# Kernel optimization log

Measured on AMD Instinct MI355X. Metric: run time of the kernel, lower is better.

Reference implementation:

```python
import jax, jax.numpy as jnp
import numpy as np

HIDDEN = 1024
FFN = 4096
N_EXPERTS = 8
TOP_K = 2


def setup_inputs() -> dict:
    key = jax.random.key(0)
    ks = jax.random.split(key, 6)
    x = jax.random.normal(ks[0], (2, 2048, HIDDEN), dtype=jnp.float32)
    Wr = jax.random.normal(ks[1], (N_EXPERTS, HIDDEN), dtype=jnp.float32) * 0.02
    W1 = jax.random.normal(ks[2], (N_EXPERTS, FFN, HIDDEN), dtype=jnp.float32) * 0.02
    b1 = jnp.zeros((N_EXPERTS, FFN), dtype=jnp.float32)
    W2 = jax.random.normal(ks[3], (N_EXPERTS, HIDDEN, FFN), dtype=jnp.float32) * 0.02
    b2 = jnp.zeros((N_EXPERTS, HIDDEN), dtype=jnp.float32)
    return {"x": x, "Wr": Wr, "W1": W1, "b1": b1, "W2": W2, "b2": b2}


def reference(x, Wr, W1, b1, W2, b2):
    # x: [B, S, D]; Wr: [E, D]; W1: [E, F, D]; W2: [E, D, F]
    B, S, D = x.shape
    E = Wr.shape[0]
    xf = x.reshape(-1, D)                              # [T, D]
    T = xf.shape[0]
    logits = xf @ Wr.T                                 # [T, E]
    probs = jax.nn.softmax(logits, axis=-1)
    top_v, top_i = jax.lax.top_k(probs, TOP_K)         # [T, K]
    top_v = top_v / jnp.sum(top_v, axis=-1, keepdims=True)
    # combine weights: zero except the top-k experts per token
    comb = jnp.zeros((T, E), dtype=xf.dtype).at[jnp.arange(T)[:, None], top_i].add(top_v)
    # run every expert densely (same math as gather/FFN/weighted-scatter)
    h = jax.nn.gelu(jnp.einsum('td,efd->etf', xf, W1) + b1[:, None, :], approximate=False)  # [E, T, F]
    y = jnp.einsum('etf,edf->etd', h, W2) + b2[:, None, :]                                   # [E, T, D]
    out = jnp.einsum('etd,te->td', y, comb)            # weighted combine
    return out.reshape(B, S, D)
```

## Files before the change

### kernel.cpp

```cpp
#include <hip/hip_runtime.h>

#define HIDDEN 1024
#define FFN    4096
#define NEXP   8
#define TOKENS 4096
#define ASSIGN 8192
#define NENT   72

typedef __attribute__((ext_vector_type(8))) short s8v;
typedef __attribute__((ext_vector_type(4))) float f4v;

__device__ __forceinline__ float bf2f(ushort u) {
    return __uint_as_float(((unsigned int)u) << 16);
}
__device__ __forceinline__ ushort f2bf(float f) {
    unsigned int x = __float_as_uint(f);
    return (ushort)((x + 0x7fffu + ((x >> 16) & 1u)) >> 16);
}

__device__ __forceinline__ float gelu_f(float v) {
    const float u = v * 0.70710678118654752f;
    const float a = fabsf(u);
    const float t = 1.0f / fmaf(0.3275911f, a, 1.0f);
    const float p = t * (0.254829592f + t * (-0.284496736f + t * (1.421413741f +
                     t * (-1.453152027f + t * 1.061405429f))));
    const float ex = __expf(-u * u);
    float er = 1.0f - p * ex;
    er = (u < 0.f) ? -er : er;
    return 0.5f * v * (1.0f + er);
}

#define GLDS16(g, l) __builtin_amdgcn_global_load_lds( \
    (const __attribute__((address_space(1))) unsigned int*)(g), \
    (__attribute__((address_space(3))) unsigned int*)(l), 16, 0, 0)

__device__ __forceinline__ int swz_scol(int t) {
    const int srow = t >> 2, c = t & 3;
    return ((c ^ ((srow >> 1) & 3)) << 3);
}
__device__ __forceinline__ int lds_off(int row, int lq) {
    return row * 32 + ((lq ^ ((row >> 1) & 3)) << 3);
}

#define KBODY(it, bA, bB, sA, sB)                                               \
  {                                                                             \
    if ((it) == NT - 1)      { asm volatile("s_waitcnt vmcnt(0)" ::: "memory");}\
    else if ((it) == NT - 2) { asm volatile("s_waitcnt vmcnt(4)" ::: "memory");}\
    else                     { asm volatile("s_waitcnt vmcnt(8)" ::: "memory");}\
    __builtin_amdgcn_s_barrier();                                               \
    __builtin_amdgcn_sched_barrier(0);                                          \
    if ((it) + 3 < NT) {                                                        \
      const int kn_ = ((it) + 3) * 32;                                          \
      GLDS16(gA0 + kn_, (sA) + wv * 512);                                       \
      GLDS16(gA1 + kn_, (sA) + 2048 + wv * 512);                                \
      GLDS16(gB0 + kn_, (sB) + wv * 512);                                       \
      GLDS16(gB1 + kn_, (sB) + 2048 + wv * 512);                                \
    }                                                                           \
    s8v a_[4], b_[4];                                                           \
    _Pragma("unroll")                                                           \
    for (int i_ = 0; i_ < 4; ++i_)                                              \
      a_[i_] = *(const s8v*)((bA) + lds_off(row_off + i_ * 16 + l15, lq));      \
    _Pragma("unroll")                                                           \
    for (int j_ = 0; j_ < 4; ++j_)                                              \
      b_[j_] = *(const s8v*)((bB) + lds_off(col_off + j_ * 16 + l15, lq));      \
    __builtin_amdgcn_s_setprio(1);                                              \
    _Pragma("unroll")                                                           \
    for (int i_ = 0; i_ < 4; ++i_)                                              \
      _Pragma("unroll")                                                         \
      for (int j_ = 0; j_ < 4; ++j_)                                            \
        acc[i_][j_] = __builtin_amdgcn_mfma_f32_16x16x32_bf16(a_[i_], b_[j_],   \
                                                              acc[i_][j_], 0, 0, 0); \
    __builtin_amdgcn_s_setprio(0);                                              \
  }

__global__ void conv_kernel(const float4* __restrict__ src, ushort4* __restrict__ dst) {
    const int i = blockIdx.x * blockDim.x + threadIdx.x;
    const float4 v = src[i];
    ushort4 o;
    o.x = f2bf(v.x); o.y = f2bf(v.y); o.z = f2bf(v.z); o.w = f2bf(v.w);
    dst[i] = o;
}

__global__ void router_kernel(const float* __restrict__ x, const float* __restrict__ Wr,
                              int* __restrict__ counts, int* __restrict__ topk_idx,
                              float* __restrict__ topk_w) {
    const int tok  = blockIdx.x;
    const int lane = threadIdx.x;
    float acc[NEXP];
#pragma unroll
    for (int e = 0; e < NEXP; ++e) acc[e] = 0.f;
#pragma unroll
    for (int i = 0; i < HIDDEN / 64; ++i) {
        const int idx = i * 64 + lane;
        const float xv = x[(size_t)tok * HIDDEN + idx];
#pragma unroll
        for (int e = 0; e < NEXP; ++e) acc[e] += xv * Wr[e * HIDDEN + idx];
    }
#pragma unroll
    for (int e = 0; e < NEXP; ++e) {
#pragma unroll
        for (int off = 32; off > 0; off >>= 1) acc[e] += __shfl_xor(acc[e], off);
    }
    if (lane == 0) {
        int i0 = 0;
        for (int e = 1; e < NEXP; ++e) if (acc[e] > acc[i0]) i0 = e;
        int i1 = (i0 == 0) ? 1 : 0;
        for (int e = 0; e < NEXP; ++e) if (e != i0 && acc[e] > acc[i1]) i1 = e;
        const float e1 = expf(acc[i1] - acc[i0]);
        const float s  = 1.f + e1;
        topk_idx[tok * 2 + 0] = i0;
        topk_idx[tok * 2 + 1] = i1;
        topk_w[tok * 2 + 0]   = 1.f / s;
        topk_w[tok * 2 + 1]   = e1 / s;
        atomicAdd(&counts[i0], 1);
        atomicAdd(&counts[i1], 1);
    }
}

__global__ void prefix_kernel(const int* __restrict__ counts, int* __restrict__ offsets,
                              int* __restrict__ cursors, int* __restrict__ tiles) {
    if (threadIdx.x == 0) {
        int s = 0, nt = 0;
        for (int e = 0; e < NEXP; ++e) {
            offsets[e] = s; cursors[e] = s;
            const int ne = counts[e];
            for (int tm = 0; tm * 128 < ne; ++tm) tiles[nt++] = e | (tm << 8);
            s += ne;
        }
        offsets[NEXP] = s;
        for (; nt < NENT; ++nt) tiles[nt] = -1;
    }
}

__global__ void scatter_kernel(const int* __restrict__ topk_idx, const float* __restrict__ topk_w,
                               int* __restrict__ cursors, int* __restrict__ token_list,
                               float* __restrict__ weight_list) {
    const int a = blockIdx.x * blockDim.x + threadIdx.x;
    if (a >= ASSIGN) return;
    const int e   = topk_idx[a];
    const int pos = atomicAdd(&cursors[e], 1);
    token_list[pos]  = a >> 1;
    weight_list[pos] = topk_w[a];
}

__global__ __launch_bounds__(256)
void gemm1_kernel(const ushort* __restrict__ x, const ushort* __restrict__ W1,
                  const float* __restrict__ b1, const int* __restrict__ token_list,
                  const int* __restrict__ counts, const int* __restrict__ offsets,
                  const int* __restrict__ tiles, ushort* __restrict__ h) {
    const int info = tiles[blockIdx.x];
    if (info < 0) return;
    const int e      = info & 255;
    const int tile_m = info >> 8;
    const int tile_n = blockIdx.y;
    const int n_e    = counts[e];
    const int base   = offsets[e];

    __shared__ __align__(16) ushort As[4 * 128 * 32];
    __shared__ __align__(16) ushort Bs[4 * 128 * 32];

    const int t    = threadIdx.x;
    const int lane = t & 63;
    const int wv   = t >> 6;
    const int srow = t >> 2;
    const int scol = swz_scol(t);

    const int r0 = tile_m * 128 + srow;
    const int r1 = r0 + 64;
    const int tokA0 = token_list[base + (r0 < n_e ? r0 : n_e - 1)];
    const int tokA1 = token_list[base + (r1 < n_e ? r1 : n_e - 1)];
    const ushort* gA0 = x + (size_t)tokA0 * HIDDEN + scol;
    const ushort* gA1 = x + (size_t)tokA1 * HIDDEN + scol;
    const ushort* gB0 = W1 + ((size_t)e * FFN + tile_n * 128 + srow) * HIDDEN + scol;
    const ushort* gB1 = W1 + ((size_t)e * FFN + tile_n * 128 + 64 + srow) * HIDDEN + scol;

    f4v acc[4][4];
#pragma unroll
    for (int i = 0; i < 4; ++i)
#pragma unroll
        for (int j = 0; j < 4; ++j) { f4v z = {0.f, 0.f, 0.f, 0.f}; acc[i][j] = z; }

    const int row_off = (wv & 1) * 64;
    const int col_off = (wv >> 1) * 64;
    const int l15 = lane & 15;
    const int lq  = lane >> 4;

    const int NT = HIDDEN / 32;

#pragma unroll
    for (int p = 0; p < 3; ++p) {
        GLDS16(gA0 + p * 32, As + p * 4096 + wv * 512);
        GLDS16(gA1 + p * 32, As + p * 4096 + 2048 + wv * 512);
        GLDS16(gB0 + p * 32, Bs + p * 4096 + wv * 512);
        GLDS16(gB1 + p * 32, Bs + p * 4096 + 2048 + wv * 512);
    }

    for (int it0 = 0; it0 < NT; it0 += 4) {
        KBODY(it0 + 0, As + 0 * 4096, Bs + 0 * 4096, As + 3 * 4096, Bs + 3 * 4096);
        KBODY(it0 + 1, As + 1 * 4096, Bs + 1 * 4096, As + 0 * 4096, Bs + 0 * 4096);
        KBODY(it0 + 2, As + 2 * 4096, Bs + 2 * 4096, As + 1 * 4096, Bs + 1 * 4096);
        KBODY(it0 + 3, As + 3 * 4096, Bs + 3 * 4096, As + 2 * 4096, Bs + 2 * 4096);
    }

    const int mrem = n_e - tile_m * 128;
#pragma unroll
    for (int i = 0; i < 4; ++i) {
#pragma unroll
        for (int rr = 0; rr < 4; ++rr) {
            const int m_loc = row_off + i * 16 + lq * 4 + rr;
            if (m_loc < mrem) {
                const size_t hrow = (size_t)(base + tile_m * 128 + m_loc) * FFN;
#pragma unroll
                for (int j = 0; j < 4; ++j) {
                    const int colF = tile_n * 128 + col_off + j * 16 + l15;
                    const float v = gelu_f(acc[i][j][rr] + b1[e * FFN + colF]);
                    h[hrow + colF] = f2bf(v);
                }
            }
        }
    }
}

__global__ __launch_bounds__(256)
void gemm2_kernel(const ushort* __restrict__ h, const ushort* __restrict__ W2,
                  const float* __restrict__ b2, const float* __restrict__ weight_list,
                  const int* __restrict__ token_list, const int* __restrict__ counts,
                  const int* __restrict__ offsets, const int* __restrict__ tiles,
                  float* __restrict__ out) {
    const int info = tiles[blockIdx.x];
    if (info < 0) return;
    const int e      = info & 255;
    const int tile_m = info >> 8;
    const int tile_n = blockIdx.y;
    const int n_e    = counts[e];
    const int base   = offsets[e];

    __shared__ __align__(16) ushort As[4 * 128 * 32];
    __shared__ __align__(16) ushort Bs[4 * 128 * 32];

    const int t    = threadIdx.x;
    const int lane = t & 63;
    const int wv   = t >> 6;
    const int srow = t >> 2;
    const int scol = swz_scol(t);

    const int r0 = tile_m * 128 + srow;
    const int r1 = r0 + 64;
    const int slot0 = base + (r0 < n_e ? r0 : n_e - 1);
    const int slot1 = base + (r1 < n_e ? r1 : n_e - 1);
    const ushort* gA0 = h + (size_t)slot0 * FFN + scol;
    const ushort* gA1 = h + (size_t)slot1 * FFN + scol;
    const ushort* gB0 = W2 + ((size_t)e * HIDDEN + tile_n * 128 + srow) * FFN + scol;
    const ushort* gB1 = W2 + ((size_t)e * HIDDEN + tile_n * 128 + 64 + srow) * FFN + scol;

    f4v acc[4][4];
#pragma unroll
    for (int i = 0; i < 4; ++i)
#pragma unroll
        for (int j = 0; j < 4; ++j) { f4v z = {0.f, 0.f, 0.f, 0.f}; acc[i][j] = z; }

    const int row_off = (wv & 1) * 64;
    const int col_off = (wv >> 1) * 64;
    const int l15 = lane & 15;
    const int lq  = lane >> 4;

    const int NT = FFN / 32;

#pragma unroll
    for (int p = 0; p < 3; ++p) {
        GLDS16(gA0 + p * 32, As + p * 4096 + wv * 512);
        GLDS16(gA1 + p * 32, As + p * 4096 + 2048 + wv * 512);
        GLDS16(gB0 + p * 32, Bs + p * 4096 + wv * 512);
        GLDS16(gB1 + p * 32, Bs + p * 4096 + 2048 + wv * 512);
    }

    for (int it0 = 0; it0 < NT; it0 += 4) {
        KBODY(it0 + 0, As + 0 * 4096, Bs + 0 * 4096, As + 3 * 4096, Bs + 3 * 4096);
        KBODY(it0 + 1, As + 1 * 4096, Bs + 1 * 4096, As + 0 * 4096, Bs + 0 * 4096);
        KBODY(it0 + 2, As + 2 * 4096, Bs + 2 * 4096, As + 1 * 4096, Bs + 1 * 4096);
        KBODY(it0 + 3, As + 3 * 4096, Bs + 3 * 4096, As + 2 * 4096, Bs + 2 * 4096);
    }

    const int mrem = n_e - tile_m * 128;
#pragma unroll
    for (int i = 0; i < 4; ++i) {
#pragma unroll
        for (int rr = 0; rr < 4; ++rr) {
            const int m_loc = row_off + i * 16 + lq * 4 + rr;
            if (m_loc < mrem) {
                const int slot  = base + tile_m * 128 + m_loc;
                const float wgt = weight_list[slot];
                const int   tok = token_list[slot];
#pragma unroll
                for (int j = 0; j < 4; ++j) {
                    const int colD = tile_n * 128 + col_off + j * 16 + l15;
                    const float v = acc[i][j][rr] + b2[e * HIDDEN + colD];
                    atomicAdd(&out[(size_t)tok * HIDDEN + colD], v * wgt);
                }
            }
        }
    }
}

extern "C" void kernel_launch(void* const* d_in, const int* in_sizes, int n_in,
                              void* d_out, int out_size, void* d_ws, size_t ws_size,
                              hipStream_t stream) {
    const float* x  = (const float*)d_in[0];
    const float* Wr = (const float*)d_in[1];
    const float* W1 = (const float*)d_in[2];
    const float* b1 = (const float*)d_in[3];
    const float* W2 = (const float*)d_in[4];
    const float* b2 = (const float*)d_in[5];
    float* out = (float*)d_out;

    char* ws = (char*)d_ws;
    int*    counts      = (int*)(ws + 0);
    int*    offsets     = (int*)(ws + 256);
    int*    cursors     = (int*)(ws + 512);
    int*    tiles       = (int*)(ws + 768);
    int*    topk_idx    = (int*)(ws + 2048);
    float*  topk_w      = (float*)(ws + 2048 + 32768);
    int*    token_list  = (int*)(ws + 2048 + 65536);
    float*  weight_list = (float*)(ws + 2048 + 98304);
    ushort* x_bf        = (ushort*)(ws + (1 << 20));
    ushort* wbuf        = (ushort*)(ws + (1 << 20) + 8388608);
    ushort* h           = (ushort*)(ws + (1 << 20) + 8388608 + 67108864);

    const int NW = NEXP * FFN * HIDDEN;

    hipMemsetAsync(counts, 0, 64, stream);
    hipMemsetAsync(out, 0, (size_t)TOKENS * HIDDEN * 4, stream);
    conv_kernel<<<(TOKENS * HIDDEN / 4) / 256, 256, 0, stream>>>((const float4*)x, (ushort4*)x_bf);
    conv_kernel<<<(NW / 4) / 256, 256, 0, stream>>>((const float4*)W1, (ushort4*)wbuf);

    router_kernel<<<TOKENS, 64, 0, stream>>>(x, Wr, counts, topk_idx, topk_w);
    prefix_kernel<<<1, 64, 0, stream>>>(counts, offsets, cursors, tiles);
    scatter_kernel<<<ASSIGN / 256, 256, 0, stream>>>(topk_idx, topk_w, cursors,
                                                     token_list, weight_list);

    gemm1_kernel<<<dim3(NENT, FFN / 128), 256, 0, stream>>>(
        x_bf, wbuf, b1, token_list, counts, offsets, tiles, h);

    conv_kernel<<<(NW / 4) / 256, 256, 0, stream>>>((const float4*)W2, (ushort4*)wbuf);

    gemm2_kernel<<<dim3(NENT, HIDDEN / 128), 256, 0, stream>>>(
        h, wbuf, b2, weight_list, token_list, counts, offsets, tiles, out);
}
```

Baseline: 811.6 us.

## Enlarge GEMM tiles to 256 rows, replace atomic combine with bf16 staging

```diff
diff --git a/kernel.cpp b/kernel.cpp
--- a/kernel.cpp
+++ b/kernel.cpp
@@ -5,7 +5,7 @@
 #define NEXP   8
 #define TOKENS 4096
 #define ASSIGN 8192
-#define NENT   72
+#define NENT   40
 
 typedef __attribute__((ext_vector_type(8))) short s8v;
 typedef __attribute__((ext_vector_type(4))) float f4v;
@@ -35,43 +35,11 @@
     (__attribute__((address_space(3))) unsigned int*)(l), 16, 0, 0)
 
 __device__ __forceinline__ int swz_scol(int t) {
-    const int srow = t >> 2, c = t & 3;
-    return ((c ^ ((srow >> 1) & 3)) << 3);
+    return (((t & 3) ^ ((t >> 3) & 3)) << 3);
 }
 __device__ __forceinline__ int lds_off(int row, int lq) {
     return row * 32 + ((lq ^ ((row >> 1) & 3)) << 3);
 }
-
-#define KBODY(it, bA, bB, sA, sB)                                               \
-  {                                                                             \
-    if ((it) == NT - 1)      { asm volatile("s_waitcnt vmcnt(0)" ::: "memory");}\
-    else if ((it) == NT - 2) { asm volatile("s_waitcnt vmcnt(4)" ::: "memory");}\
-    else                     { asm volatile("s_waitcnt vmcnt(8)" ::: "memory");}\
-    __builtin_amdgcn_s_barrier();                                               \
-    __builtin_amdgcn_sched_barrier(0);                                          \
-    if ((it) + 3 < NT) {                                                        \
-      const int kn_ = ((it) + 3) * 32;                                          \
-      GLDS16(gA0 + kn_, (sA) + wv * 512);                                       \
-      GLDS16(gA1 + kn_, (sA) + 2048 + wv * 512);                                \
-      GLDS16(gB0 + kn_, (sB) + wv * 512);                                       \
-      GLDS16(gB1 + kn_, (sB) + 2048 + wv * 512);                                \
-    }                                                                           \
-    s8v a_[4], b_[4];                                                           \
-    _Pragma("unroll")                                                           \
-    for (int i_ = 0; i_ < 4; ++i_)                                              \
-      a_[i_] = *(const s8v*)((bA) + lds_off(row_off + i_ * 16 + l15, lq));      \
-    _Pragma("unroll")                                                           \
-    for (int j_ = 0; j_ < 4; ++j_)                                              \
-      b_[j_] = *(const s8v*)((bB) + lds_off(col_off + j_ * 16 + l15, lq));      \
-    __builtin_amdgcn_s_setprio(1);                                              \
-    _Pragma("unroll")                                                           \
-    for (int i_ = 0; i_ < 4; ++i_)                                              \
-      _Pragma("unroll")                                                         \
-      for (int j_ = 0; j_ < 4; ++j_)                                            \
-        acc[i_][j_] = __builtin_amdgcn_mfma_f32_16x16x32_bf16(a_[i_], b_[j_],   \
-                                                              acc[i_][j_], 0, 0, 0); \
-    __builtin_amdgcn_s_setprio(0);                                              \
-  }
 
 __global__ void conv_kernel(const float4* __restrict__ src, ushort4* __restrict__ dst) {
     const int i = blockIdx.x * blockDim.x + threadIdx.x;
@@ -83,7 +51,7 @@
 
 __global__ void router_kernel(const float* __restrict__ x, const float* __restrict__ Wr,
                               int* __restrict__ counts, int* __restrict__ topk_idx,
-                              float* __restrict__ topk_w) {
+                              float* __restrict__ topk_w, ushort* __restrict__ x_bf) {
     const int tok  = blockIdx.x;
     const int lane = threadIdx.x;
     float acc[NEXP];
@@ -93,6 +61,7 @@
     for (int i = 0; i < HIDDEN / 64; ++i) {
         const int idx = i * 64 + lane;
         const float xv = x[(size_t)tok * HIDDEN + idx];
+        x_bf[(size_t)tok * HIDDEN + idx] = f2bf(xv);
 #pragma unroll
         for (int e = 0; e < NEXP; ++e) acc[e] += xv * Wr[e * HIDDEN + idx];
     }
@@ -124,7 +93,7 @@
         for (int e = 0; e < NEXP; ++e) {
             offsets[e] = s; cursors[e] = s;
             const int ne = counts[e];
-            for (int tm = 0; tm * 128 < ne; ++tm) tiles[nt++] = e | (tm << 8);
+            for (int tm = 0; tm * 256 < ne; ++tm) tiles[nt++] = e | (tm << 8);
             s += ne;
         }
         offsets[NEXP] = s;
@@ -134,85 +103,127 @@
 
 __global__ void scatter_kernel(const int* __restrict__ topk_idx, const float* __restrict__ topk_w,
                                int* __restrict__ cursors, int* __restrict__ token_list,
-                               float* __restrict__ weight_list) {
+                               float* __restrict__ weight_list, int* __restrict__ slot_of) {
     const int a = blockIdx.x * blockDim.x + threadIdx.x;
     if (a >= ASSIGN) return;
     const int e   = topk_idx[a];
     const int pos = atomicAdd(&cursors[e], 1);
     token_list[pos]  = a >> 1;
     weight_list[pos] = topk_w[a];
-}
-
-__global__ __launch_bounds__(256)
+    slot_of[a]       = pos;
+}
+
+#define G1_TILE(T, CA, CB, SA, SB)                                              \
+  if ((T) < NT) {                                                               \
+    if ((T) + 2 < NT) {                                                         \
+      const int kn_ = ((T) + 2) * 32;                                           \
+      GLDS16(gA0 + kn_, (SA) + wv * 512);                                       \
+      GLDS16(gA1 + kn_, (SA) + 4096 + wv * 512);                                \
+      GLDS16(gB0 + kn_, (SB) + wv * 512);                                       \
+      GLDS16(gB1 + kn_, (SB) + 4096 + wv * 512);                                \
+    }                                                                           \
+    s8v a_[4], b_[4], c_[4];                                                    \
+    _Pragma("unroll")                                                           \
+    for (int i_ = 0; i_ < 4; ++i_)                                              \
+      a_[i_] = *(const s8v*)((CA) + lds_off(wm * 128 + i_ * 16 + l15, lq));     \
+    _Pragma("unroll")                                                           \
+    for (int j_ = 0; j_ < 4; ++j_)                                              \
+      b_[j_] = *(const s8v*)((CB) + lds_off(wn * 64 + j_ * 16 + l15, lq));      \
+    _Pragma("unroll")                                                           \
+    for (int i_ = 0; i_ < 4; ++i_)                                              \
+      c_[i_] = *(const s8v*)((CA) + lds_off(wm * 128 + 64 + i_ * 16 + l15, lq));\
+    __builtin_amdgcn_s_setprio(1);                                              \
+    _Pragma("unroll")                                                           \
+    for (int i_ = 0; i_ < 4; ++i_)                                              \
+      _Pragma("unroll")                                                         \
+      for (int j_ = 0; j_ < 4; ++j_)                                            \
+        acc[i_][j_] = __builtin_amdgcn_mfma_f32_16x16x32_bf16(a_[i_], b_[j_],   \
+                                                              acc[i_][j_], 0, 0, 0); \
+    _Pragma("unroll")                                                           \
+    for (int i_ = 0; i_ < 4; ++i_)                                              \
+      _Pragma("unroll")                                                         \
+      for (int j_ = 0; j_ < 4; ++j_)                                            \
+        acc[4 + i_][j_] = __builtin_amdgcn_mfma_f32_16x16x32_bf16(c_[i_], b_[j_], \
+                                                              acc[4 + i_][j_], 0, 0, 0); \
+    __builtin_amdgcn_s_setprio(0);                                              \
+    if ((T) >= NT - 2) { asm volatile("s_waitcnt vmcnt(0)" ::: "memory"); }     \
+    else               { asm volatile("s_waitcnt vmcnt(4)" ::: "memory"); }     \
+    __builtin_amdgcn_s_barrier();                                               \
+    __builtin_amdgcn_sched_barrier(0);                                          \
+  }
+
+__global__ __launch_bounds__(512, 2)
 void gemm1_kernel(const ushort* __restrict__ x, const ushort* __restrict__ W1,
                   const float* __restrict__ b1, const int* __restrict__ token_list,
                   const int* __restrict__ counts, const int* __restrict__ offsets,
                   const int* __restrict__ tiles, ushort* __restrict__ h) {
-    const int info = tiles[blockIdx.x];
+    const int info = tiles[blockIdx.y];
     if (info < 0) return;
     const int e      = info & 255;
     const int tile_m = info >> 8;
-    const int tile_n = blockIdx.y;
+    const int tile_n = blockIdx.x;
     const int n_e    = counts[e];
     const int base   = offsets[e];
 
-    __shared__ __align__(16) ushort As[4 * 128 * 32];
-    __shared__ __align__(16) ushort Bs[4 * 128 * 32];
+    __shared__ __align__(16) ushort As[3 * 256 * 32];
+    __shared__ __align__(16) ushort Bs[3 * 256 * 32];
 
     const int t    = threadIdx.x;
+    const int wv   = t >> 6;
     const int lane = t & 63;
-    const int wv   = t >> 6;
     const int srow = t >> 2;
     const int scol = swz_scol(t);
 
-    const int r0 = tile_m * 128 + srow;
-    const int r1 = r0 + 64;
+    const int r0 = tile_m * 256 + srow;
+    const int r1 = r0 + 128;
     const int tokA0 = token_list[base + (r0 < n_e ? r0 : n_e - 1)];
     const int tokA1 = token_list[base + (r1 < n_e ? r1 : n_e - 1)];
     const ushort* gA0 = x + (size_t)tokA0 * HIDDEN + scol;
     const ushort* gA1 = x + (size_t)tokA1 * HIDDEN + scol;
-    const ushort* gB0 = W1 + ((size_t)e * FFN + tile_n * 128 + srow) * HIDDEN + scol;
-    const ushort* gB1 = W1 + ((size_t)e * FFN + tile_n * 128 + 64 + srow) * HIDDEN + scol;
-
-    f4v acc[4][4];
-#pragma unroll
-    for (int i = 0; i < 4; ++i)
+    const ushort* gB0 = W1 + ((size_t)e * FFN + tile_n * 256 + srow) * HIDDEN + scol;
+    const ushort* gB1 = W1 + ((size_t)e * FFN + tile_n * 256 + 128 + srow) * HIDDEN + scol;
+
+    f4v acc[8][4];
+#pragma unroll
+    for (int i = 0; i < 8; ++i)
 #pragma unroll
         for (int j = 0; j < 4; ++j) { f4v z = {0.f, 0.f, 0.f, 0.f}; acc[i][j] = z; }
 
-    const int row_off = (wv & 1) * 64;
-    const int col_off = (wv >> 1) * 64;
+    const int wm  = wv >> 2;
+    const int wn  = wv & 3;
     const int l15 = lane & 15;
     const int lq  = lane >> 4;
 
     const int NT = HIDDEN / 32;
 
 #pragma unroll
-    for (int p = 0; p < 3; ++p) {
-        GLDS16(gA0 + p * 32, As + p * 4096 + wv * 512);
-        GLDS16(gA1 + p * 32, As + p * 4096 + 2048 + wv * 512);
-        GLDS16(gB0 + p * 32, Bs + p * 4096 + wv * 512);
-        GLDS16(gB1 + p * 32, Bs + p * 4096 + 2048 + wv * 512);
-    }
-
-    for (int it0 = 0; it0 < NT; it0 += 4) {
-        KBODY(it0 + 0, As + 0 * 4096, Bs + 0 * 4096, As + 3 * 4096, Bs + 3 * 4096);
-        KBODY(it0 + 1, As + 1 * 4096, Bs + 1 * 4096, As + 0 * 4096, Bs + 0 * 4096);
-        KBODY(it0 + 2, As + 2 * 4096, Bs + 2 * 4096, As + 1 * 4096, Bs + 1 * 4096);
-        KBODY(it0 + 3, As + 3 * 4096, Bs + 3 * 4096, As + 2 * 4096, Bs + 2 * 4096);
-    }
-
-    const int mrem = n_e - tile_m * 128;
-#pragma unroll
-    for (int i = 0; i < 4; ++i) {
+    for (int p = 0; p < 2; ++p) {
+        GLDS16(gA0 + p * 32, As + p * 8192 + wv * 512);
+        GLDS16(gA1 + p * 32, As + p * 8192 + 4096 + wv * 512);
+        GLDS16(gB0 + p * 32, Bs + p * 8192 + wv * 512);
+        GLDS16(gB1 + p * 32, Bs + p * 8192 + 4096 + wv * 512);
+    }
+    asm volatile("s_waitcnt vmcnt(4)" ::: "memory");
+    __builtin_amdgcn_s_barrier();
+    __builtin_amdgcn_sched_barrier(0);
+
+    for (int t0 = 0; t0 < NT; t0 += 3) {
+        G1_TILE(t0 + 0, As + 0 * 8192, Bs + 0 * 8192, As + 2 * 8192, Bs + 2 * 8192);
+        G1_TILE(t0 + 1, As + 1 * 8192, Bs + 1 * 8192, As + 0 * 8192, Bs + 0 * 8192);
+        G1_TILE(t0 + 2, As + 2 * 8192, Bs + 2 * 8192, As + 1 * 8192, Bs + 1 * 8192);
+    }
+
+    const int mrem = n_e - tile_m * 256;
+#pragma unroll
+    for (int i = 0; i < 8; ++i) {
 #pragma unroll
         for (int rr = 0; rr < 4; ++rr) {
-            const int m_loc = row_off + i * 16 + lq * 4 + rr;
+            const int m_loc = wm * 128 + i * 16 + lq * 4 + rr;
             if (m_loc < mrem) {
-                const size_t hrow = (size_t)(base + tile_m * 128 + m_loc) * FFN;
+                const size_t hrow = (size_t)(base + tile_m * 256 + m_loc) * FFN;
 #pragma unroll
                 for (int j = 0; j < 4; ++j) {
-                    const int colF = tile_n * 128 + col_off + j * 16 + l15;
+                    const int colF = tile_n * 256 + wn * 64 + j * 16 + l15;
                     const float v = gelu_f(acc[i][j][rr] + b1[e * FFN + colF]);
                     h[hrow + colF] = f2bf(v);
                 }
@@ -221,85 +232,138 @@
     }
 }
 
-__global__ __launch_bounds__(256)
+#define G2_TILE(T, CA, CB, SA, SB)                                              \
+  if ((T) < NT) {                                                               \
+    if ((T) + 2 < NT) {                                                         \
+      const int kn_ = ((T) + 2) * 32;                                           \
+      GLDS16(gA0 + kn_, (SA) + wv * 512);                                       \
+      GLDS16(gA1 + kn_, (SA) + 4096 + wv * 512);                                \
+      GLDS16(gB0 + kn_, (SB) + wv * 512);                                       \
+    }                                                                           \
+    s8v a_[4], b_[2], c_[4];                                                    \
+    _Pragma("unroll")                                                           \
+    for (int i_ = 0; i_ < 4; ++i_)                                              \
+      a_[i_] = *(const s8v*)((CA) + lds_off(wm * 128 + i_ * 16 + l15, lq));     \
+    _Pragma("unroll")                                                           \
+    for (int j_ = 0; j_ < 2; ++j_)                                              \
+      b_[j_] = *(const s8v*)((CB) + lds_off(wn * 32 + j_ * 16 + l15, lq));      \
+    _Pragma("unroll")                                                           \
+    for (int i_ = 0; i_ < 4; ++i_)                                              \
+      c_[i_] = *(const s8v*)((CA) + lds_off(wm * 128 + 64 + i_ * 16 + l15, lq));\
+    __builtin_amdgcn_s_setprio(1);                                              \
+    _Pragma("unroll")                                                           \
+    for (int i_ = 0; i_ < 4; ++i_)                                              \
+      _Pragma("unroll")                                                         \
+      for (int j_ = 0; j_ < 2; ++j_)                                            \
+        acc[i_][j_] = __builtin_amdgcn_mfma_f32_16x16x32_bf16(a_[i_], b_[j_],   \
+                                                              acc[i_][j_], 0, 0, 0); \
+    _Pragma("unroll")                                                           \
+    for (int i_ = 0; i_ < 4; ++i_)                                              \
+      _Pragma("unroll")                                                         \
+      for (int j_ = 0; j_ < 2; ++j_)                                            \
+        acc[4 + i_][j_] = __builtin_amdgcn_mfma_f32_16x16x32_bf16(c_[i_], b_[j_], \
+                                                              acc[4 + i_][j_], 0, 0, 0); \
+    __builtin_amdgcn_s_setprio(0);                                              \
+    if ((T) >= NT - 2) { asm volatile("s_waitcnt vmcnt(0)" ::: "memory"); }     \
+    else               { asm volatile("s_waitcnt vmcnt(3)" ::: "memory"); }     \
+    __builtin_amdgcn_s_barrier();                                               \
+    __builtin_amdgcn_sched_barrier(0);                                          \
+  }
+
+__global__ __launch_bounds__(512, 2)
 void gemm2_kernel(const ushort* __restrict__ h, const ushort* __restrict__ W2,
                   const float* __restrict__ b2, const float* __restrict__ weight_list,
-                  const int* __restrict__ token_list, const int* __restrict__ counts,
-                  const int* __restrict__ offsets, const int* __restrict__ tiles,
-                  float* __restrict__ out) {
-    const int info = tiles[blockIdx.x];
+                  const int* __restrict__ counts, const int* __restrict__ offsets,
+                  const int* __restrict__ tiles, ushort* __restrict__ y) {
+    const int info = tiles[blockIdx.y];
     if (info < 0) return;
     const int e      = info & 255;
     const int tile_m = info >> 8;
-    const int tile_n = blockIdx.y;
+    const int tile_n = blockIdx.x;
     const int n_e    = counts[e];
     const int base   = offsets[e];
 
-    __shared__ __align__(16) ushort As[4 * 128 * 32];
-    __shared__ __align__(16) ushort Bs[4 * 128 * 32];
+    __shared__ __align__(16) ushort As[3 * 256 * 32];
+    __shared__ __align__(16) ushort Bs[3 * 128 * 32];
 
     const int t    = threadIdx.x;
+    const int wv   = t >> 6;
     const int lane = t & 63;
-    const int wv   = t >> 6;
     const int srow = t >> 2;
     const int scol = swz_scol(t);
 
-    const int r0 = tile_m * 128 + srow;
-    const int r1 = r0 + 64;
+    const int r0 = tile_m * 256 + srow;
+    const int r1 = r0 + 128;
     const int slot0 = base + (r0 < n_e ? r0 : n_e - 1);
     const int slot1 = base + (r1 < n_e ? r1 : n_e - 1);
     const ushort* gA0 = h + (size_t)slot0 * FFN + scol;
     const ushort* gA1 = h + (size_t)slot1 * FFN + scol;
     const ushort* gB0 = W2 + ((size_t)e * HIDDEN + tile_n * 128 + srow) * FFN + scol;
-    const ushort* gB1 = W2 + ((size_t)e * HIDDEN + tile_n * 128 + 64 + srow) * FFN + scol;
-
-    f4v acc[4][4];
-#pragma unroll
-    for (int i = 0; i < 4; ++i)
-#pragma unroll
-        for (int j = 0; j < 4; ++j) { f4v z = {0.f, 0.f, 0.f, 0.f}; acc[i][j] = z; }
-
-    const int row_off = (wv & 1) * 64;
-    const int col_off = (wv >> 1) * 64;
+
+    f4v acc[8][2];
+#pragma unroll
+    for (int i = 0; i < 8; ++i)
+#pragma unroll
+        for (int j = 0; j < 2; ++j) { f4v z = {0.f, 0.f, 0.f, 0.f}; acc[i][j] = z; }
+
+    const int wm  = wv >> 2;
+    const int wn  = wv & 3;
     const int l15 = lane & 15;
     const int lq  = lane >> 4;
 
     const int NT = FFN / 32;
 
 #pragma unroll
-    for (int p = 0; p < 3; ++p) {
-        GLDS16(gA0 + p * 32, As + p * 4096 + wv * 512);
-        GLDS16(gA1 + p * 32, As + p * 4096 + 2048 + wv * 512);
+    for (int p = 0; p < 2; ++p) {
+        GLDS16(gA0 + p * 32, As + p * 8192 + wv * 512);
+        GLDS16(gA1 + p * 32, As + p * 8192 + 4096 + wv * 512);
         GLDS16(gB0 + p * 32, Bs + p * 4096 + wv * 512);
-        GLDS16(gB1 + p * 32, Bs + p * 4096 + 2048 + wv * 512);
-    }
-
-    for (int it0 = 0; it0 < NT; it0 += 4) {
-        KBODY(it0 + 0, As + 0 * 4096, Bs + 0 * 4096, As + 3 * 4096, Bs + 3 * 4096);
-        KBODY(it0 + 1, As + 1 * 4096, Bs + 1 * 4096, As + 0 * 4096, Bs + 0 * 4096);
-        KBODY(it0 + 2, As + 2 * 4096, Bs + 2 * 4096, As + 1 * 4096, Bs + 1 * 4096);
-        KBODY(it0 + 3, As + 3 * 4096, Bs + 3 * 4096, As + 2 * 4096, Bs + 2 * 4096);
-    }
-
-    const int mrem = n_e - tile_m * 128;
-#pragma unroll
-    for (int i = 0; i < 4; ++i) {
+    }
+    asm volatile("s_waitcnt vmcnt(3)" ::: "memory");
+    __builtin_amdgcn_s_barrier();
+    __builtin_amdgcn_sched_barrier(0);
+
+    for (int t0 = 0; t0 < NT; t0 += 3) {
+        G2_TILE(t0 + 0, As + 0 * 8192, Bs + 0 * 4096, As + 2 * 8192, Bs + 2 * 4096);
+        G2_TILE(t0 + 1, As + 1 * 8192, Bs + 1 * 4096, As + 0 * 8192, Bs + 0 * 4096);
+        G2_TILE(t0 + 2, As + 2 * 8192, Bs + 2 * 4096, As + 1 * 8192, Bs + 1 * 4096);
+    }
+
+    const int mrem = n_e - tile_m * 256;
+#pragma unroll
+    for (int i = 0; i < 8; ++i) {
 #pragma unroll
         for (int rr = 0; rr < 4; ++rr) {
-            const int m_loc = row_off + i * 16 + lq * 4 + rr;
+            const int m_loc = wm * 128 + i * 16 + lq * 4 + rr;
             if (m_loc < mrem) {
-                const int slot  = base + tile_m * 128 + m_loc;
+                const int slot  = base + tile_m * 256 + m_loc;
                 const float wgt = weight_list[slot];
-                const int   tok = token_list[slot];
-#pragma unroll
-                for (int j = 0; j < 4; ++j) {
-                    const int colD = tile_n * 128 + col_off + j * 16 + l15;
+#pragma unroll
+                for (int j = 0; j < 2; ++j) {
+                    const int colD = tile_n * 128 + wn * 32 + j * 16 + l15;
                     const float v = acc[i][j][rr] + b2[e * HIDDEN + colD];
-                    atomicAdd(&out[(size_t)tok * HIDDEN + colD], v * wgt);
+                    y[(size_t)slot * HIDDEN + colD] = f2bf(v * wgt);
                 }
             }
         }
     }
+}
+
+__global__ void combine_kernel(const int* __restrict__ slot_of, const ushort* __restrict__ y,
+                               float* __restrict__ out) {
+    const int idx = blockIdx.x * blockDim.x + threadIdx.x;
+    const int t = idx >> 8;
+    const int d = (idx & 255) * 4;
+    const int s0 = slot_of[t * 2 + 0];
+    const int s1 = slot_of[t * 2 + 1];
+    const ushort4 a = *(const ushort4*)(y + (size_t)s0 * HIDDEN + d);
+    const ushort4 b = *(const ushort4*)(y + (size_t)s1 * HIDDEN + d);
+    float4 o;
+    o.x = bf2f(a.x) + bf2f(b.x);
+    o.y = bf2f(a.y) + bf2f(b.y);
+    o.z = bf2f(a.z) + bf2f(b.z);
+    o.w = bf2f(a.w) + bf2f(b.w);
+    *(float4*)(out + (size_t)t * HIDDEN + d) = o;
 }
 
 extern "C" void kernel_launch(void* const* d_in, const int* in_sizes, int n_in,
@@ -320,29 +384,31 @@
     int*    tiles       = (int*)(ws + 768);
     int*    topk_idx    = (int*)(ws + 2048);
     float*  topk_w      = (float*)(ws + 2048 + 32768);
-    int*    token_list  = (int*)(ws + 2048 + 65536);
-    float*  weight_list = (float*)(ws + 2048 + 98304);
+    int*    slot_of     = (int*)(ws + 2048 + 65536);
+    int*    token_list  = (int*)(ws + 2048 + 98304);
+    float*  weight_list = (float*)(ws + 2048 + 131072);
     ushort* x_bf        = (ushort*)(ws + (1 << 20));
     ushort* wbuf        = (ushort*)(ws + (1 << 20) + 8388608);
     ushort* h           = (ushort*)(ws + (1 << 20) + 8388608 + 67108864);
+    ushort* y           = (ushort*)(ws + (1 << 20) + 8388608 + 2 * 67108864ull);
 
     const int NW = NEXP * FFN * HIDDEN;
 
     hipMemsetAsync(counts, 0, 64, stream);
-    hipMemsetAsync(out, 0, (size_t)TOKENS * HIDDEN * 4, stream);
-    conv_kernel<<<(TOKENS * HIDDEN / 4) / 256, 256, 0, stream>>>((const float4*)x, (ushort4*)x_bf);
+    router_kernel<<<TOKENS, 64, 0, stream>>>(x, Wr, counts, topk_idx, topk_w, x_bf);
     conv_kernel<<<(NW / 4) / 256, 256, 0, stream>>>((const float4*)W1, (ushort4*)wbuf);
 
-    router_kernel<<<TOKENS, 64, 0, stream>>>(x, Wr, counts, topk_idx, topk_w);
     prefix_kernel<<<1, 64, 0, stream>>>(counts, offsets, cursors, tiles);
     scatter_kernel<<<ASSIGN / 256, 256, 0, stream>>>(topk_idx, topk_w, cursors,
-                                                     token_list, weight_list);
-
-    gemm1_kernel<<<dim3(NENT, FFN / 128), 256, 0, stream>>>(
+                                                     token_list, weight_list, slot_of);
+
+    gemm1_kernel<<<dim3(FFN / 256, NENT), 512, 0, stream>>>(
         x_bf, wbuf, b1, token_list, counts, offsets, tiles, h);
 
     conv_kernel<<<(NW / 4) / 256, 256, 0, stream>>>((const float4*)W2, (ushort4*)wbuf);
 
-    gemm2_kernel<<<dim3(NENT, HIDDEN / 128), 256, 0, stream>>>(
-        h, wbuf, b2, weight_list, token_list, counts, offsets, tiles, out);
-}
+    gemm2_kernel<<<dim3(HIDDEN / 128, NENT), 512, 0, stream>>>(
+        h, wbuf, b2, weight_list, counts, offsets, tiles, y);
+
+    combine_kernel<<<(TOKENS * HIDDEN / 4) / 256, 256, 0, stream>>>(slot_of, y, out);
+}
```

New measurement: 706.5 us. -13.0%, faster.
